# Kernel optimization log

Hardware: AMD Instinct MI355X
Metric: run time of the kernel (lower is better)

## Reference

```python
import jax, jax.numpy as jnp
import numpy as np

N, G, C, A, E = 10000, 12, 64, 3, 50000
LN_EPS = 1e-5


def setup_inputs() -> dict:
    key = jax.random.key(0)
    ks = jax.random.split(key, 12)
    s = 0.05
    return {
        "x": jax.random.normal(ks[0], (N, G, C), jnp.float32),
        "edge_attr": jax.random.normal(ks[1], (E, G, G, A), jnp.float32),
        "W_kernel": jax.random.normal(ks[2], (A, C), jnp.float32) * s,   # depthwise kernel basis Linear(attr_dim->C)
        "conv_bias": jax.random.normal(ks[3], (C,), jnp.float32) * s,
        "ln_w": jnp.ones((C,), jnp.float32),
        "ln_b": jnp.zeros((C,), jnp.float32),
        "W1": jax.random.normal(ks[4], (C, C), jnp.float32) * s,          # stored [in,out]
        "b1": jax.random.normal(ks[5], (C,), jnp.float32) * s,
        "W2": jax.random.normal(ks[6], (C, C), jnp.float32) * s,
        "b2": jax.random.normal(ks[7], (C,), jnp.float32) * s,
        "layer_scale": jnp.full((1, C), 1e-6, jnp.float32),
        "edge_index": jax.random.randint(ks[8], (2, E), 0, N, jnp.int32),
        "batch": jnp.zeros((N,), jnp.int32),
    }


def reference(x, edge_attr, W_kernel, conv_bias, ln_w, ln_b, W1, b1, W2, b2,
              layer_scale, edge_index, batch):
    src, dst = edge_index[0], edge_index[1]
    x_j = x[src]                                            # [E,G,C] gather
    # depthwise fiber conv: m[e,g,c] = sum_{h,a} attr[e,g,h,a] * Wk[a,c] * x_j[e,h,c]
    # contract over source grid h first to avoid materializing the [E,G,G,C] kernel
    t = jnp.einsum('egha,ehc->egac', edge_attr, x_j)        # [E,G,A,C]
    m = jnp.einsum('egac,ac->egc', t, W_kernel)             # [E,G,C]
    agg = jnp.zeros_like(x).at[dst].add(m) + conv_bias      # scatter-add, [N,G,C]
    # LayerNorm over channel dim
    mu = jnp.mean(agg, axis=-1, keepdims=True)
    var = jnp.mean(jnp.square(agg - mu), axis=-1, keepdims=True)
    h = (agg - mu) * jax.lax.rsqrt(var + LN_EPS) * ln_w + ln_b
    # 2-layer MLP with exact GELU (torch default)
    h = jax.nn.gelu(h @ W1 + b1, approximate=False) @ W2 + b2
    h = layer_scale * h                                     # broadcast [1,C] over [N,G,C]
    return x + h                                            # residual (same shape)
```

## Files before the change

kernel.cpp:

```cpp
#include <hip/hip_runtime.h>
#include <math.h>

#define NN 10000
#define GG 12
#define CC 64
#define AA 3
#define EE 50000
#define LN_EPS 1e-5f
#define MAXDEG 64

typedef __attribute__((ext_vector_type(4))) float f4;
typedef __attribute__((ext_vector_type(4))) short s4;

union S4U { s4 s; unsigned int w[2]; };
union I2S { int i[2]; s4 s; };

__device__ __forceinline__ s4 pack4(float k0, float k1, float k2, float k3) {
    S4U t;
    t.w[0] = __builtin_amdgcn_perm(__float_as_uint(k1), __float_as_uint(k0), 0x07060302u);
    t.w[1] = __builtin_amdgcn_perm(__float_as_uint(k3), __float_as_uint(k2), 0x07060302u);
    return t.s;
}
__device__ __forceinline__ unsigned int pack2(float a, float b) {
    return __builtin_amdgcn_perm(__float_as_uint(b), __float_as_uint(a), 0x07060302u);
}

__device__ __forceinline__ f4 mfma_bf16(s4 a, s4 b, f4 c) {
#if __has_builtin(__builtin_amdgcn_mfma_f32_16x16x16bf16_1k)
    return __builtin_amdgcn_mfma_f32_16x16x16bf16_1k(a, b, c, 0, 0, 0);
#else
    asm volatile("v_mfma_f32_16x16x16_bf16 %0, %1, %2, %0" : "+v"(c) : "v"(a), "v"(b));
    return c;
#endif
}

__global__ __launch_bounds__(256) void xpack(const float* __restrict__ x,
                                             unsigned int* __restrict__ xp,
                                             int* __restrict__ cnt) {
    const int gid = blockIdx.x * 256 + threadIdx.x;
    if (gid < NN) cnt[gid] = 0;

    const int l  = threadIdx.x & 63;
    const int n  = blockIdx.x * 4 + (threadIdx.x >> 6);
    const int lm = l & 15;
    const int lg = l >> 4;

    unsigned int d[8];
    if (lg < 3) {
        const char* xb = (const char*)(x + n * (GG * CC)) + lg * 1024 + lm * 4;
#pragma unroll
        for (int t = 0; t < 4; ++t) {
            const float v0 = *(const float*)(xb + t * 64 + 0 * 256);
            const float v1 = *(const float*)(xb + t * 64 + 1 * 256);
            const float v2 = *(const float*)(xb + t * 64 + 2 * 256);
            const float v3 = *(const float*)(xb + t * 64 + 3 * 256);
            d[2 * t]     = pack2(v0, v1);
            d[2 * t + 1] = pack2(v2, v3);
        }
    } else {
#pragma unroll
        for (int k = 0; k < 8; ++k) d[k] = 0u;
    }
    unsigned int* o = xp + (size_t)n * 512 + l * 8;
    *(uint4*)o       = make_uint4(d[0], d[1], d[2], d[3]);
    *(uint4*)(o + 4) = make_uint4(d[4], d[5], d[6], d[7]);
}

__global__ __launch_bounds__(256) void bucket_fill(const int* __restrict__ ei,
                                                   int* __restrict__ cnt,
                                                   int* __restrict__ elist) {
    int e = blockIdx.x * 256 + threadIdx.x;
    if (e < EE) {
        int src = ei[e];
        int dst = ei[EE + e];
        int pos = atomicAdd(&cnt[dst], 1);
        if (pos < MAXDEG) elist[dst * MAXDEG + pos] = e | (src << 17);
    }
}

__global__ __launch_bounds__(256) void conv_fused(
    const unsigned int* __restrict__ xp, const float* __restrict__ attr,
    const float* __restrict__ Wk,  const float* __restrict__ cb,
    const float* __restrict__ lnw, const float* __restrict__ lnb,
    const float* __restrict__ W1,  const float* __restrict__ b1,
    const float* __restrict__ W2,  const float* __restrict__ b2,
    const float* __restrict__ ls,  const float* __restrict__ x,
    const int* __restrict__ cnt,   const int* __restrict__ elist,
    float* __restrict__ out) {
    __shared__ float scratch[4][1088];

    const int l  = threadIdx.x & 63;
    const int w  = threadIdx.x >> 6;
    const int n  = blockIdx.x * 4 + w;
    const int lm = l & 15;
    const int lg = l >> 4;

    const int fbase = (lm < 12 && lg < 3) ? (lm * 36 + lg * 12) : 0;
    const int a1l   = (l < 44) ? l : 43;

    const int deg = min(cnt[n], MAXDEG);
    const int myE = elist[n * MAXDEG + l];

    float wk[3][4];
#pragma unroll
    for (int a = 0; a < 3; ++a)
#pragma unroll
        for (int t = 0; t < 4; ++t)
            wk[a][t] = Wk[a * CC + lm + 16 * t];

    f4 acc[3][4];
#pragma unroll
    for (int a = 0; a < 3; ++a)
#pragma unroll
        for (int t = 0; t < 4; ++t) acc[a][t] = (f4){0.f, 0.f, 0.f, 0.f};

    f4 Aa0, Aa1, Ab0, Ab1;
    int4 Xa0, Xa1, Xb0, Xb1;

#define LOADE(idx, A0, A1, X0, X1)                                              \
    {                                                                           \
        const int p = __builtin_amdgcn_readlane(myE, (idx));                    \
        const char* ab = (const char*)(attr + (size_t)(p & 0x1FFFF) * 432);     \
        A0 = *(const f4*)(ab + 16 * l);                                         \
        A1 = *(const f4*)(ab + 1024 + 16 * a1l);                                \
        const int* xb = (const int*)(xp + (size_t)(p >> 17) * 512 + 8 * l);     \
        X0 = *(const int4*)xb;                                                  \
        X1 = *(const int4*)(xb + 4);                                            \
    }

#define STAGE(slot, A0, A1)                                                     \
    {                                                                           \
        float* sw = &scratch[w][(slot) * 432];                                  \
        *(f4*)(sw + 4 * l) = A0;                                                \
        if (l < 44) *(f4*)(sw + 256 + 4 * l) = A1;                              \
    }

#define COMPUTE(slot, X0, X1)                                                   \
    {                                                                           \
        I2S u0, u1, u2, u3;                                                     \
        u0.i[0] = X0.x; u0.i[1] = X0.y;                                         \
        u1.i[0] = X0.z; u1.i[1] = X0.w;                                         \
        u2.i[0] = X1.x; u2.i[1] = X1.y;                                         \
        u3.i[0] = X1.z; u3.i[1] = X1.w;                                         \
        const float* sr = &scratch[w][(slot) * 432] + fbase;                    \
        const f4 q0 = *(const f4*)(sr);                                         \
        const f4 q1 = *(const f4*)(sr + 4);                                     \
        const f4 q2 = *(const f4*)(sr + 8);                                     \
        const s4 af0 = pack4(q0[0], q0[3], q1[2], q2[1]);                       \
        const s4 af1 = pack4(q0[1], q1[0], q1[3], q2[2]);                       \
        const s4 af2 = pack4(q0[2], q1[1], q2[0], q2[3]);                       \
        acc[0][0] = mfma_bf16(af0, u0.s, acc[0][0]);                            \
        acc[1][0] = mfma_bf16(af1, u0.s, acc[1][0]);                            \
        acc[2][0] = mfma_bf16(af2, u0.s, acc[2][0]);                            \
        acc[0][1] = mfma_bf16(af0, u1.s, acc[0][1]);                            \
        acc[1][1] = mfma_bf16(af1, u1.s, acc[1][1]);                            \
        acc[2][1] = mfma_bf16(af2, u1.s, acc[2][1]);                            \
        acc[0][2] = mfma_bf16(af0, u2.s, acc[0][2]);                            \
        acc[1][2] = mfma_bf16(af1, u2.s, acc[1][2]);                            \
        acc[2][2] = mfma_bf16(af2, u2.s, acc[2][2]);                            \
        acc[0][3] = mfma_bf16(af0, u3.s, acc[0][3]);                            \
        acc[1][3] = mfma_bf16(af1, u3.s, acc[1][3]);                            \
        acc[2][3] = mfma_bf16(af2, u3.s, acc[2][3]);                            \
    }

    if (deg > 0) LOADE(0, Aa0, Aa1, Xa0, Xa1);
    if (deg > 1) LOADE(1, Ab0, Ab1, Xb0, Xb1);
    if (deg > 0) STAGE(0, Aa0, Aa1);

    for (int j = 0; j < deg; j += 2) {
        COMPUTE(0, Xa0, Xa1);
        if (j + 2 < deg) LOADE(j + 2, Aa0, Aa1, Xa0, Xa1);
        if (j + 1 < deg) {
            STAGE(1, Ab0, Ab1);
            COMPUTE(1, Xb0, Xb1);
            if (j + 3 < deg) LOADE(j + 3, Ab0, Ab1, Xb0, Xb1);
            if (j + 2 < deg) STAGE(0, Aa0, Aa1);
        }
    }

#undef LOADE
#undef STAGE
#undef COMPUTE

    float* hb = &scratch[w][0];

    if (lg < 3) {
#pragma unroll
        for (int t = 0; t < 4; ++t) {
            const float cbT = cb[lm + 16 * t];
#pragma unroll
            for (int r = 0; r < 4; ++r) {
                const float mv = fmaf(acc[0][t][r], wk[0][t],
                                 fmaf(acc[1][t][r], wk[1][t],
                                      acc[2][t][r] * wk[2][t])) + cbT;
                hb[(4 * lg + r) * 68 + lm + 16 * t] = mv;
            }
        }
    }
    *(f4*)(hb + (12 + lg) * 68 + 4 * lm) = (f4){0.f, 0.f, 0.f, 0.f};

    f4 h4[4];
#pragma unroll
    for (int kt = 0; kt < 4; ++kt)
        h4[kt] = *(const f4*)(hb + lm * 68 + 4 * lg + 16 * kt);

    f4 lw4[4], lb4[4];
#pragma unroll
    for (int kt = 0; kt < 4; ++kt) {
        lw4[kt] = *(const f4*)(lnw + 4 * lg + 16 * kt);
        lb4[kt] = *(const f4*)(lnb + 4 * lg + 16 * kt);
    }

    float s = 0.f, s2 = 0.f;
#pragma unroll
    for (int kt = 0; kt < 4; ++kt)
#pragma unroll
        for (int j = 0; j < 4; ++j) {
            const float v = h4[kt][j];
            s += v; s2 += v * v;
        }
    s  += __shfl_xor(s, 16);  s  += __shfl_xor(s, 32);
    s2 += __shfl_xor(s2, 16); s2 += __shfl_xor(s2, 32);
    const float mu  = s * (1.f / 64.f);
    const float inv = rsqrtf(s2 * (1.f / 64.f) - mu * mu + LN_EPS);

    s4 hf[4];
#pragma unroll
    for (int kt = 0; kt < 4; ++kt) {
        const float n0 = (h4[kt][0] - mu) * inv * lw4[kt][0] + lb4[kt][0];
        const float n1 = (h4[kt][1] - mu) * inv * lw4[kt][1] + lb4[kt][1];
        const float n2 = (h4[kt][2] - mu) * inv * lw4[kt][2] + lb4[kt][2];
        const float n3 = (h4[kt][3] - mu) * inv * lw4[kt][3] + lb4[kt][3];
        hf[kt] = pack4(n0, n1, n2, n3);
    }

    f4 z[4];
#pragma unroll
    for (int mt = 0; mt < 4; ++mt) z[mt] = (f4){0.f, 0.f, 0.f, 0.f};
#pragma unroll
    for (int mt = 0; mt < 4; ++mt)
#pragma unroll
        for (int kt = 0; kt < 4; ++kt) {
            const int kb = 4 * lg + 16 * kt;
            const int m  = lm + 16 * mt;
            const s4 wf = pack4(W1[(kb + 0) * CC + m], W1[(kb + 1) * CC + m],
                                W1[(kb + 2) * CC + m], W1[(kb + 3) * CC + m]);
            z[mt] = mfma_bf16(wf, hf[kt], z[mt]);
        }

    s4 gf[4];
#pragma unroll
    for (int mt = 0; mt < 4; ++mt) {
        const f4 b14 = *(const f4*)(b1 + 16 * mt + 4 * lg);
        float g[4];
#pragma unroll
        for (int r = 0; r < 4; ++r) {
            const float zz = z[mt][r] + b14[r];
            g[r] = 0.5f * zz * (1.f + erff(zz * 0.70710678118654752f));
        }
        gf[mt] = pack4(g[0], g[1], g[2], g[3]);
    }

    f4 o[4];
#pragma unroll
    for (int mt = 0; mt < 4; ++mt) o[mt] = (f4){0.f, 0.f, 0.f, 0.f};
#pragma unroll
    for (int mt = 0; mt < 4; ++mt)
#pragma unroll
        for (int kt = 0; kt < 4; ++kt) {
            const int kb = 4 * lg + 16 * kt;
            const int m  = lm + 16 * mt;
            const s4 wf = pack4(W2[(kb + 0) * CC + m], W2[(kb + 1) * CC + m],
                                W2[(kb + 2) * CC + m], W2[(kb + 3) * CC + m]);
            o[mt] = mfma_bf16(wf, gf[kt], o[mt]);
        }

    const int fb2 = lm * 68;
    const int swz = (l & 7) << 2;
#pragma unroll
    for (int mt = 0; mt < 4; ++mt)
#pragma unroll
        for (int r = 0; r < 4; ++r)
            hb[fb2 + ((16 * mt + 4 * lg + r) ^ swz)] = o[mt][r];

    const f4 b2q = *(const f4*)(b2 + 4 * lm);
    const f4 lsq = *(const f4*)(ls + 4 * lm);
    const int f0 = n * GG;

#pragma unroll
    for (int rr = 0; rr < 3; ++rr) {
        const int R   = rr * 4 + lg;
        const int col = 4 * lm;
        const f4 ov = *(const f4*)(&hb[R * 68 + (col ^ ((R & 7) << 2))]);
        const f4 xv = *(const f4*)(x + (size_t)(f0 + R) * CC + col);
        f4 res;
#pragma unroll
        for (int k = 0; k < 4; ++k)
            res[k] = fmaf(lsq[k], ov[k] + b2q[k], xv[k]);
        *(f4*)(out + (size_t)(f0 + R) * CC + col) = res;
    }
}

extern "C" void kernel_launch(void* const* d_in, const int* in_sizes, int n_in,
                              void* d_out, int out_size, void* d_ws, size_t ws_size,
                              hipStream_t stream) {
    const float* x    = (const float*)d_in[0];
    const float* attr = (const float*)d_in[1];
    const float* Wk   = (const float*)d_in[2];
    const float* cb   = (const float*)d_in[3];
    const float* lnw  = (const float*)d_in[4];
    const float* lnb  = (const float*)d_in[5];
    const float* W1   = (const float*)d_in[6];
    const float* b1   = (const float*)d_in[7];
    const float* W2   = (const float*)d_in[8];
    const float* b2   = (const float*)d_in[9];
    const float* ls   = (const float*)d_in[10];
    const int*   ei   = (const int*)d_in[11];
    float* out = (float*)d_out;

    int* cnt   = (int*)d_ws;
    int* elist = cnt + NN;
    unsigned int* xp = (unsigned int*)(elist + NN * MAXDEG);

    xpack<<<NN / 4, 256, 0, stream>>>(x, xp, cnt);
    bucket_fill<<<(EE + 255) / 256, 256, 0, stream>>>(ei, cnt, elist);
    conv_fused<<<NN / 4, 256, 0, stream>>>(xp, attr, Wk, cb, lnw, lnb, W1, b1,
                                           W2, b2, ls, x, cnt, elist, out);
}
```

Before: 69.61 us.

## Sort nodes by degree for load balance and restructure edge loop into 3-edge chunks

Adds histogram, prefix and scatter kernels that build a node ordering sorted by descending in-degree. The fused conv kernel then processes nodes in that order, so the four waves in a block have similar edge counts and the heaviest nodes are scheduled first. The edge loop is also changed from a 2-stage software pipeline to chunks that issue up to three edge loads before computing. The cost is three extra small kernel launches, including a serial single-thread prefix, plus scattered output and x accesses from the permuted node order.

Measured after the change: 156.7 us. 125% more time.

```diff
diff --git a/kernel.cpp b/kernel.cpp
--- a/kernel.cpp
+++ b/kernel.cpp
@@ -36,9 +36,11 @@
 
 __global__ __launch_bounds__(256) void xpack(const float* __restrict__ x,
                                              unsigned int* __restrict__ xp,
-                                             int* __restrict__ cnt) {
+                                             int* __restrict__ cnt,
+                                             int* __restrict__ hist) {
     const int gid = blockIdx.x * 256 + threadIdx.x;
     if (gid < NN) cnt[gid] = 0;
+    if (gid < 2 * (MAXDEG + 1)) hist[gid] = 0;
 
     const int l  = threadIdx.x & 63;
     const int n  = blockIdx.x * 4 + (threadIdx.x >> 6);
@@ -78,6 +80,28 @@
     }
 }
 
+__global__ __launch_bounds__(256) void deg_hist(const int* __restrict__ cnt,
+                                                int* __restrict__ hist) {
+    int n = blockIdx.x * 256 + threadIdx.x;
+    if (n < NN) atomicAdd(&hist[min(cnt[n], MAXDEG)], 1);
+}
+__global__ __launch_bounds__(64) void deg_prefix(const int* __restrict__ hist,
+                                                 int* __restrict__ off) {
+    if (threadIdx.x == 0) {
+        int acc = 0;
+        for (int d = MAXDEG; d >= 0; --d) { off[d] = acc; acc += hist[d]; }
+    }
+}
+__global__ __launch_bounds__(256) void deg_scatter(const int* __restrict__ cnt,
+                                                   int* __restrict__ off,
+                                                   int* __restrict__ nord) {
+    int n = blockIdx.x * 256 + threadIdx.x;
+    if (n < NN) {
+        int pos = atomicAdd(&off[min(cnt[n], MAXDEG)], 1);
+        nord[pos] = n;
+    }
+}
+
 __global__ __launch_bounds__(256) void conv_fused(
     const unsigned int* __restrict__ xp, const float* __restrict__ attr,
     const float* __restrict__ Wk,  const float* __restrict__ cb,
@@ -86,12 +110,13 @@
     const float* __restrict__ W2,  const float* __restrict__ b2,
     const float* __restrict__ ls,  const float* __restrict__ x,
     const int* __restrict__ cnt,   const int* __restrict__ elist,
+    const int* __restrict__ nord,
     float* __restrict__ out) {
     __shared__ float scratch[4][1088];
 
     const int l  = threadIdx.x & 63;
     const int w  = threadIdx.x >> 6;
-    const int n  = blockIdx.x * 4 + w;
+    const int n  = nord[blockIdx.x * 4 + w];
     const int lm = l & 15;
     const int lg = l >> 4;
 
@@ -114,8 +139,8 @@
 #pragma unroll
         for (int t = 0; t < 4; ++t) acc[a][t] = (f4){0.f, 0.f, 0.f, 0.f};
 
-    f4 Aa0, Aa1, Ab0, Ab1;
-    int4 Xa0, Xa1, Xb0, Xb1;
+    f4 Aa0, Aa1, Ab0, Ab1, Ac0, Ac1;
+    int4 Xa0, Xa1, Xb0, Xb1, Xc0, Xc1;
 
 #define LOADE(idx, A0, A1, X0, X1)                                              \
     {                                                                           \
@@ -163,24 +188,31 @@
         acc[2][3] = mfma_bf16(af2, u3.s, acc[2][3]);                            \
     }
 
-    if (deg > 0) LOADE(0, Aa0, Aa1, Xa0, Xa1);
-    if (deg > 1) LOADE(1, Ab0, Ab1, Xb0, Xb1);
-    if (deg > 0) STAGE(0, Aa0, Aa1);
-
-    for (int j = 0; j < deg; j += 2) {
-        COMPUTE(0, Xa0, Xa1);
-        if (j + 2 < deg) LOADE(j + 2, Aa0, Aa1, Xa0, Xa1);
-        if (j + 1 < deg) {
-            STAGE(1, Ab0, Ab1);
-            COMPUTE(1, Xb0, Xb1);
-            if (j + 3 < deg) LOADE(j + 3, Ab0, Ab1, Xb0, Xb1);
-            if (j + 2 < deg) STAGE(0, Aa0, Aa1);
-        }
+#define CH1(i) { LOADE((i),Aa0,Aa1,Xa0,Xa1);                                    \
+                 STAGE(0,Aa0,Aa1); COMPUTE(0,Xa0,Xa1); }
+#define CH2(i) { LOADE((i),Aa0,Aa1,Xa0,Xa1); LOADE((i)+1,Ab0,Ab1,Xb0,Xb1);      \
+                 STAGE(0,Aa0,Aa1); COMPUTE(0,Xa0,Xa1);                          \
+                 STAGE(1,Ab0,Ab1); COMPUTE(1,Xb0,Xb1); }
+#define CH3(i) { LOADE((i),Aa0,Aa1,Xa0,Xa1); LOADE((i)+1,Ab0,Ab1,Xb0,Xb1);      \
+                 LOADE((i)+2,Ac0,Ac1,Xc0,Xc1);                                  \
+                 STAGE(0,Aa0,Aa1); COMPUTE(0,Xa0,Xa1);                          \
+                 STAGE(1,Ab0,Ab1); COMPUTE(1,Xb0,Xb1);                          \
+                 STAGE(0,Ac0,Ac1); COMPUTE(0,Xc0,Xc1); }
+
+    int i = 0;
+    while (i < deg) {
+        const int c = deg - i;
+        if (c >= 3)      { CH3(i); i += 3; }
+        else if (c == 2) { CH2(i); i += 2; }
+        else             { CH1(i); i += 1; }
     }
 
 #undef LOADE
 #undef STAGE
 #undef COMPUTE
+#undef CH1
+#undef CH2
+#undef CH3
 
     float* hb = &scratch[w][0];
 
@@ -321,9 +353,15 @@
     int* cnt   = (int*)d_ws;
     int* elist = cnt + NN;
     unsigned int* xp = (unsigned int*)(elist + NN * MAXDEG);
-
-    xpack<<<NN / 4, 256, 0, stream>>>(x, xp, cnt);
+    int* hist  = (int*)(xp + (size_t)NN * 512);
+    int* off   = hist + (MAXDEG + 1);
+    int* nord  = off + (MAXDEG + 1);
+
+    xpack<<<NN / 4, 256, 0, stream>>>(x, xp, cnt, hist);
     bucket_fill<<<(EE + 255) / 256, 256, 0, stream>>>(ei, cnt, elist);
+    deg_hist<<<(NN + 255) / 256, 256, 0, stream>>>(cnt, hist);
+    deg_prefix<<<1, 64, 0, stream>>>(hist, off);
+    deg_scatter<<<(NN + 255) / 256, 256, 0, stream>>>(cnt, off, nord);
     conv_fused<<<NN / 4, 256, 0, stream>>>(xp, attr, Wk, cb, lnw, lnb, W1, b1,
-                                           W2, b2, ls, x, cnt, elist, out);
-}
+                                           W2, b2, ls, x, cnt, elist, nord, out);
+}
```

## Stream edge attr and packed x directly to LDS with triple-buffered async loads

Applied to the files above, without the earlier changes.

Replaces the register-staged double-buffered gather (global loads into VGPRs, then ds_write to LDS) with global_load_lds direct-to-LDS copies into a three-slot ring per wave. The loop paces itself with explicit vmcnt waits and prefetches up to three edges ahead. The aim is to drop the VGPR round-trip and LDS store instructions and to hide gather latency with deeper prefetch. In exchange, LDS per block grows from about 17 KB to 48 KB, which may lower occupancy, and correctness now relies on hand-written waitcnt counts matching the number of issued loads.

Measured after the change: 69.83 us. Within noise of the previous version (+0.3%).

```diff
diff --git a/kernel.cpp b/kernel.cpp
--- a/kernel.cpp
+++ b/kernel.cpp
@@ -32,6 +32,12 @@
     asm volatile("v_mfma_f32_16x16x16_bf16 %0, %1, %2, %0" : "+v"(c) : "v"(a), "v"(b));
     return c;
 #endif
+}
+
+__device__ __forceinline__ void gll(const void* g, void* s) {
+    __builtin_amdgcn_global_load_lds(
+        (const __attribute__((address_space(1))) void*)g,
+        (__attribute__((address_space(3))) void*)s, 16, 0, 0);
 }
 
 __global__ __launch_bounds__(256) void xpack(const float* __restrict__ x,
@@ -87,7 +93,7 @@
     const float* __restrict__ ls,  const float* __restrict__ x,
     const int* __restrict__ cnt,   const int* __restrict__ elist,
     float* __restrict__ out) {
-    __shared__ float scratch[4][1088];
+    __shared__ float lsa[4][3][1024];
 
     const int l  = threadIdx.x & 63;
     const int w  = threadIdx.x >> 6;
@@ -101,6 +107,73 @@
     const int deg = min(cnt[n], MAXDEG);
     const int myE = elist[n * MAXDEG + l];
 
+    f4 acc[3][4];
+#pragma unroll
+    for (int a = 0; a < 3; ++a)
+#pragma unroll
+        for (int t = 0; t < 4; ++t) acc[a][t] = (f4){0.f, 0.f, 0.f, 0.f};
+
+#define ISSUE(idx, s)                                                           \
+    {                                                                           \
+        const int p = __builtin_amdgcn_readlane(myE, (idx));                    \
+        const char* ab = (const char*)attr + (size_t)(p & 0x1FFFF) * 1728;      \
+        const char* xb = (const char*)xp + (size_t)(p >> 17) * 2048;            \
+        char* sw = (char*)&lsa[w][s][0];                                        \
+        gll(ab + 16 * l,            sw);                                        \
+        gll(ab + 1024 + 16 * a1l,   sw + 1024);                                 \
+        gll(xb + 32 * l,            sw + 2048);                                 \
+        gll(xb + 32 * l + 16,       sw + 3072);                                 \
+    }
+
+    if (deg > 0) ISSUE(0, 0);
+    if (deg > 1) ISSUE(1, 1);
+    if (deg > 2) ISSUE(2, 2);
+
+    int s = 0;
+    for (int i = 0; i < deg; ++i) {
+        const int ahead = deg - 1 - i;
+        if (ahead >= 2)      asm volatile("s_waitcnt vmcnt(8)" ::: "memory");
+        else if (ahead == 1) asm volatile("s_waitcnt vmcnt(4)" ::: "memory");
+        else                 asm volatile("s_waitcnt vmcnt(0)" ::: "memory");
+        __builtin_amdgcn_sched_barrier(0);
+
+        const float* sr = &lsa[w][s][0];
+        const f4 q0 = *(const f4*)(sr + fbase);
+        const f4 q1 = *(const f4*)(sr + fbase + 4);
+        const f4 q2 = *(const f4*)(sr + fbase + 8);
+        const int4 X0 = *(const int4*)((const char*)sr + 2048 + 16 * l);
+        const int4 X1 = *(const int4*)((const char*)sr + 3072 + 16 * l);
+
+        asm volatile("s_waitcnt lgkmcnt(0)" ::: "memory");
+        __builtin_amdgcn_sched_barrier(0);
+        if (i + 3 < deg) ISSUE(i + 3, s);
+
+        I2S u0, u1, u2, u3;
+        u0.i[0] = X0.x; u0.i[1] = X0.y;
+        u1.i[0] = X0.z; u1.i[1] = X0.w;
+        u2.i[0] = X1.x; u2.i[1] = X1.y;
+        u3.i[0] = X1.z; u3.i[1] = X1.w;
+        const s4 af0 = pack4(q0[0], q0[3], q1[2], q2[1]);
+        const s4 af1 = pack4(q0[1], q1[0], q1[3], q2[2]);
+        const s4 af2 = pack4(q0[2], q1[1], q2[0], q2[3]);
+        acc[0][0] = mfma_bf16(af0, u0.s, acc[0][0]);
+        acc[1][0] = mfma_bf16(af1, u0.s, acc[1][0]);
+        acc[2][0] = mfma_bf16(af2, u0.s, acc[2][0]);
+        acc[0][1] = mfma_bf16(af0, u1.s, acc[0][1]);
+        acc[1][1] = mfma_bf16(af1, u1.s, acc[1][1]);
+        acc[2][1] = mfma_bf16(af2, u1.s, acc[2][1]);
+        acc[0][2] = mfma_bf16(af0, u2.s, acc[0][2]);
+        acc[1][2] = mfma_bf16(af1, u2.s, acc[1][2]);
+        acc[2][2] = mfma_bf16(af2, u2.s, acc[2][2]);
+        acc[0][3] = mfma_bf16(af0, u3.s, acc[0][3]);
+        acc[1][3] = mfma_bf16(af1, u3.s, acc[1][3]);
+        acc[2][3] = mfma_bf16(af2, u3.s, acc[2][3]);
+
+        s = (s == 2) ? 0 : s + 1;
+    }
+
+#undef ISSUE
+
     float wk[3][4];
 #pragma unroll
     for (int a = 0; a < 3; ++a)
@@ -108,81 +181,7 @@
         for (int t = 0; t < 4; ++t)
             wk[a][t] = Wk[a * CC + lm + 16 * t];
 
-    f4 acc[3][4];
-#pragma unroll
-    for (int a = 0; a < 3; ++a)
-#pragma unroll
-        for (int t = 0; t < 4; ++t) acc[a][t] = (f4){0.f, 0.f, 0.f, 0.f};
-
-    f4 Aa0, Aa1, Ab0, Ab1;
-    int4 Xa0, Xa1, Xb0, Xb1;
-
-#define LOADE(idx, A0, A1, X0, X1)                                              \
-    {                                                                           \
-        const int p = __builtin_amdgcn_readlane(myE, (idx));                    \
-        const char* ab = (const char*)(attr + (size_t)(p & 0x1FFFF) * 432);     \
-        A0 = *(const f4*)(ab + 16 * l);                                         \
-        A1 = *(const f4*)(ab + 1024 + 16 * a1l);                                \
-        const int* xb = (const int*)(xp + (size_t)(p >> 17) * 512 + 8 * l);     \
-        X0 = *(const int4*)xb;                                                  \
-        X1 = *(const int4*)(xb + 4);                                            \
-    }
-
-#define STAGE(slot, A0, A1)                                                     \
-    {                                                                           \
-        float* sw = &scratch[w][(slot) * 432];                                  \
-        *(f4*)(sw + 4 * l) = A0;                                                \
-        if (l < 44) *(f4*)(sw + 256 + 4 * l) = A1;                              \
-    }
-
-#define COMPUTE(slot, X0, X1)                                                   \
-    {                                                                           \
-        I2S u0, u1, u2, u3;                                                     \
-        u0.i[0] = X0.x; u0.i[1] = X0.y;                                         \
-        u1.i[0] = X0.z; u1.i[1] = X0.w;                                         \
-        u2.i[0] = X1.x; u2.i[1] = X1.y;                                         \
-        u3.i[0] = X1.z; u3.i[1] = X1.w;                                         \
-        const float* sr = &scratch[w][(slot) * 432] + fbase;                    \
-        const f4 q0 = *(const f4*)(sr);                                         \
-        const f4 q1 = *(const f4*)(sr + 4);                                     \
-        const f4 q2 = *(const f4*)(sr + 8);                                     \
-        const s4 af0 = pack4(q0[0], q0[3], q1[2], q2[1]);                       \
-        const s4 af1 = pack4(q0[1], q1[0], q1[3], q2[2]);                       \
-        const s4 af2 = pack4(q0[2], q1[1], q2[0], q2[3]);                       \
-        acc[0][0] = mfma_bf16(af0, u0.s, acc[0][0]);                            \
-        acc[1][0] = mfma_bf16(af1, u0.s, acc[1][0]);                            \
-        acc[2][0] = mfma_bf16(af2, u0.s, acc[2][0]);                            \
-        acc[0][1] = mfma_bf16(af0, u1.s, acc[0][1]);                            \
-        acc[1][1] = mfma_bf16(af1, u1.s, acc[1][1]);                            \
-        acc[2][1] = mfma_bf16(af2, u1.s, acc[2][1]);                            \
-        acc[0][2] = mfma_bf16(af0, u2.s, acc[0][2]);                            \
-        acc[1][2] = mfma_bf16(af1, u2.s, acc[1][2]);                            \
-        acc[2][2] = mfma_bf16(af2, u2.s, acc[2][2]);                            \
-        acc[0][3] = mfma_bf16(af0, u3.s, acc[0][3]);                            \
-        acc[1][3] = mfma_bf16(af1, u3.s, acc[1][3]);                            \
-        acc[2][3] = mfma_bf16(af2, u3.s, acc[2][3]);                            \
-    }
-
-    if (deg > 0) LOADE(0, Aa0, Aa1, Xa0, Xa1);
-    if (deg > 1) LOADE(1, Ab0, Ab1, Xb0, Xb1);
-    if (deg > 0) STAGE(0, Aa0, Aa1);
-
-    for (int j = 0; j < deg; j += 2) {
-        COMPUTE(0, Xa0, Xa1);
-        if (j + 2 < deg) LOADE(j + 2, Aa0, Aa1, Xa0, Xa1);
-        if (j + 1 < deg) {
-            STAGE(1, Ab0, Ab1);
-            COMPUTE(1, Xb0, Xb1);
-            if (j + 3 < deg) LOADE(j + 3, Ab0, Ab1, Xb0, Xb1);
-            if (j + 2 < deg) STAGE(0, Aa0, Aa1);
-        }
-    }
-
-#undef LOADE
-#undef STAGE
-#undef COMPUTE
-
-    float* hb = &scratch[w][0];
+    float* hb = &lsa[w][0][0];
 
     if (lg < 3) {
 #pragma unroll
@@ -211,17 +210,17 @@
         lb4[kt] = *(const f4*)(lnb + 4 * lg + 16 * kt);
     }
 
-    float s = 0.f, s2 = 0.f;
+    float s1 = 0.f, s2 = 0.f;
 #pragma unroll
     for (int kt = 0; kt < 4; ++kt)
 #pragma unroll
         for (int j = 0; j < 4; ++j) {
             const float v = h4[kt][j];
-            s += v; s2 += v * v;
-        }
-    s  += __shfl_xor(s, 16);  s  += __shfl_xor(s, 32);
+            s1 += v; s2 += v * v;
+        }
+    s1 += __shfl_xor(s1, 16); s1 += __shfl_xor(s1, 32);
     s2 += __shfl_xor(s2, 16); s2 += __shfl_xor(s2, 32);
-    const float mu  = s * (1.f / 64.f);
+    const float mu  = s1 * (1.f / 64.f);
     const float inv = rsqrtf(s2 * (1.f / 64.f) - mu * mu + LN_EPS);
 
     s4 hf[4];
```

## Stream edge attrs via global_load_lds with 4-deep pipeline and prepacked MLP weights

Applied to the files above, without the earlier changes.

Edge attribute rows are now loaded straight into LDS with global_load_lds into a 5-slot ring per wave. The gather loop is restructured to keep four edges in flight, using explicit vmcnt waits, which removes the register staging and the LDS write pass. MLP weights are packed to bf16 MFMA fragments once, inside bucket_fill, so conv_fused reads ready fragments instead of repacking strided fp32 loads in every block. The change also sets a launch_bounds occupancy hint and raises LDS use to 40KB per block, which may limit occupancy. The hand-coded vmcnt counts depend on the exact number of memory ops each ISSUE emits, so correctness rests on that count.

Measured after the change: 74.50 us. 1.07x slower.

```diff
diff --git a/kernel.cpp b/kernel.cpp
--- a/kernel.cpp
+++ b/kernel.cpp
@@ -34,6 +34,12 @@
 #endif
 }
 
+__device__ __forceinline__ void gll(const void* g, void* s) {
+    __builtin_amdgcn_global_load_lds(
+        (const __attribute__((address_space(1))) void*)g,
+        (__attribute__((address_space(3))) void*)s, 16, 0, 0);
+}
+
 __global__ __launch_bounds__(256) void xpack(const float* __restrict__ x,
                                              unsigned int* __restrict__ xp,
                                              int* __restrict__ cnt) {
@@ -68,7 +74,10 @@
 
 __global__ __launch_bounds__(256) void bucket_fill(const int* __restrict__ ei,
                                                    int* __restrict__ cnt,
-                                                   int* __restrict__ elist) {
+                                                   int* __restrict__ elist,
+                                                   const float* __restrict__ W1,
+                                                   const float* __restrict__ W2,
+                                                   char* __restrict__ wtab) {
     int e = blockIdx.x * 256 + threadIdx.x;
     if (e < EE) {
         int src = ei[e];
@@ -76,18 +85,33 @@
         int pos = atomicAdd(&cnt[dst], 1);
         if (pos < MAXDEG) elist[dst * MAXDEG + pos] = e | (src << 17);
     }
-}
-
-__global__ __launch_bounds__(256) void conv_fused(
+    if (blockIdx.x < 2) {
+        const float* Ws = (blockIdx.x == 0) ? W1 : W2;
+        char* base = wtab + blockIdx.x * 8192;
+        const int l  = threadIdx.x & 63;
+        const int wv = threadIdx.x >> 6;
+        const int lm = l & 15, lg = l >> 4;
+        const int m  = lm + 16 * wv;
+#pragma unroll
+        for (int kt = 0; kt < 4; ++kt) {
+            const int kb = 4 * lg + 16 * kt;
+            const s4 f = pack4(Ws[(kb + 0) * CC + m], Ws[(kb + 1) * CC + m],
+                               Ws[(kb + 2) * CC + m], Ws[(kb + 3) * CC + m]);
+            *(s4*)(base + (wv * 4 + kt) * 512 + l * 8) = f;
+        }
+    }
+}
+
+__global__ __launch_bounds__(256, 4) void conv_fused(
     const unsigned int* __restrict__ xp, const float* __restrict__ attr,
     const float* __restrict__ Wk,  const float* __restrict__ cb,
     const float* __restrict__ lnw, const float* __restrict__ lnb,
-    const float* __restrict__ W1,  const float* __restrict__ b1,
-    const float* __restrict__ W2,  const float* __restrict__ b2,
-    const float* __restrict__ ls,  const float* __restrict__ x,
+    const char* __restrict__ wtab, const float* __restrict__ b1,
+    const float* __restrict__ b2,  const float* __restrict__ ls,
+    const float* __restrict__ x,
     const int* __restrict__ cnt,   const int* __restrict__ elist,
     float* __restrict__ out) {
-    __shared__ float scratch[4][1088];
+    __shared__ float lsa[4][5][512];
 
     const int l  = threadIdx.x & 63;
     const int w  = threadIdx.x >> 6;
@@ -101,51 +125,44 @@
     const int deg = min(cnt[n], MAXDEG);
     const int myE = elist[n * MAXDEG + l];
 
-    float wk[3][4];
+    f4 acc[3][4];
 #pragma unroll
     for (int a = 0; a < 3; ++a)
 #pragma unroll
-        for (int t = 0; t < 4; ++t)
-            wk[a][t] = Wk[a * CC + lm + 16 * t];
-
-    f4 acc[3][4];
-#pragma unroll
-    for (int a = 0; a < 3; ++a)
-#pragma unroll
         for (int t = 0; t < 4; ++t) acc[a][t] = (f4){0.f, 0.f, 0.f, 0.f};
 
-    f4 Aa0, Aa1, Ab0, Ab1;
-    int4 Xa0, Xa1, Xb0, Xb1;
-
-#define LOADE(idx, A0, A1, X0, X1)                                              \
+    int4 Xa0, Xa1, Xb0, Xb1, Xc0, Xc1, Xd0, Xd1;
+
+#define ISSUE(idx, X0, X1)                                                      \
     {                                                                           \
         const int p = __builtin_amdgcn_readlane(myE, (idx));                    \
-        const char* ab = (const char*)(attr + (size_t)(p & 0x1FFFF) * 432);     \
-        A0 = *(const f4*)(ab + 16 * l);                                         \
-        A1 = *(const f4*)(ab + 1024 + 16 * a1l);                                \
+        const char* ab = (const char*)attr + (size_t)(p & 0x1FFFF) * 1728;      \
         const int* xb = (const int*)(xp + (size_t)(p >> 17) * 512 + 8 * l);     \
+        char* sw = (char*)&lsa[w][(idx) % 5][0];                                \
+        gll(ab + 16 * l,          sw);                                          \
+        gll(ab + 1024 + 16 * a1l, sw + 1024);                                   \
         X0 = *(const int4*)xb;                                                  \
         X1 = *(const int4*)(xb + 4);                                            \
     }
 
-#define STAGE(slot, A0, A1)                                                     \
+#define EDGE(e, X0, X1)                                                         \
     {                                                                           \
-        float* sw = &scratch[w][(slot) * 432];                                  \
-        *(f4*)(sw + 4 * l) = A0;                                                \
-        if (l < 44) *(f4*)(sw + 256 + 4 * l) = A1;                              \
-    }
-
-#define COMPUTE(slot, X0, X1)                                                   \
-    {                                                                           \
+        const int ahead = deg - 1 - (e);                                        \
+        if (ahead >= 3)      asm volatile("s_waitcnt vmcnt(12)" ::: "memory");  \
+        else if (ahead == 2) asm volatile("s_waitcnt vmcnt(8)" ::: "memory");   \
+        else if (ahead == 1) asm volatile("s_waitcnt vmcnt(4)" ::: "memory");   \
+        else                 asm volatile("s_waitcnt vmcnt(0)" ::: "memory");   \
+        __builtin_amdgcn_sched_barrier(0);                                      \
+        const float* sr = &lsa[w][(e) % 5][0];                                  \
+        const f4 q0 = *(const f4*)(sr + fbase);                                 \
+        const f4 q1 = *(const f4*)(sr + fbase + 4);                             \
+        const f4 q2 = *(const f4*)(sr + fbase + 8);                             \
         I2S u0, u1, u2, u3;                                                     \
         u0.i[0] = X0.x; u0.i[1] = X0.y;                                         \
         u1.i[0] = X0.z; u1.i[1] = X0.w;                                         \
         u2.i[0] = X1.x; u2.i[1] = X1.y;                                         \
         u3.i[0] = X1.z; u3.i[1] = X1.w;                                         \
-        const float* sr = &scratch[w][(slot) * 432] + fbase;                    \
-        const f4 q0 = *(const f4*)(sr);                                         \
-        const f4 q1 = *(const f4*)(sr + 4);                                     \
-        const f4 q2 = *(const f4*)(sr + 8);                                     \
+        if ((e) + 4 < deg) ISSUE((e) + 4, X0, X1);                              \
         const s4 af0 = pack4(q0[0], q0[3], q1[2], q2[1]);                       \
         const s4 af1 = pack4(q0[1], q1[0], q1[3], q2[2]);                       \
         const s4 af2 = pack4(q0[2], q1[1], q2[0], q2[3]);                       \
@@ -163,26 +180,39 @@
         acc[2][3] = mfma_bf16(af2, u3.s, acc[2][3]);                            \
     }
 
-    if (deg > 0) LOADE(0, Aa0, Aa1, Xa0, Xa1);
-    if (deg > 1) LOADE(1, Ab0, Ab1, Xb0, Xb1);
-    if (deg > 0) STAGE(0, Aa0, Aa1);
-
-    for (int j = 0; j < deg; j += 2) {
-        COMPUTE(0, Xa0, Xa1);
-        if (j + 2 < deg) LOADE(j + 2, Aa0, Aa1, Xa0, Xa1);
-        if (j + 1 < deg) {
-            STAGE(1, Ab0, Ab1);
-            COMPUTE(1, Xb0, Xb1);
-            if (j + 3 < deg) LOADE(j + 3, Ab0, Ab1, Xb0, Xb1);
-            if (j + 2 < deg) STAGE(0, Aa0, Aa1);
-        }
-    }
-
-#undef LOADE
-#undef STAGE
-#undef COMPUTE
-
-    float* hb = &scratch[w][0];
+    if (deg > 0) ISSUE(0, Xa0, Xa1);
+    if (deg > 1) ISSUE(1, Xb0, Xb1);
+    if (deg > 2) ISSUE(2, Xc0, Xc1);
+    if (deg > 3) ISSUE(3, Xd0, Xd1);
+
+    int i = 0;
+    for (; i + 4 <= deg; i += 4) {
+        EDGE(i,     Xa0, Xa1);
+        EDGE(i + 1, Xb0, Xb1);
+        EDGE(i + 2, Xc0, Xc1);
+        EDGE(i + 3, Xd0, Xd1);
+    }
+    if (i < deg) {
+        EDGE(i, Xa0, Xa1);
+        if (i + 1 < deg) {
+            EDGE(i + 1, Xb0, Xb1);
+            if (i + 2 < deg) {
+                EDGE(i + 2, Xc0, Xc1);
+            }
+        }
+    }
+
+#undef ISSUE
+#undef EDGE
+
+    float wk[3][4];
+#pragma unroll
+    for (int a = 0; a < 3; ++a)
+#pragma unroll
+        for (int t = 0; t < 4; ++t)
+            wk[a][t] = Wk[a * CC + lm + 16 * t];
+
+    float* hb = &lsa[w][0][0];
 
     if (lg < 3) {
 #pragma unroll
@@ -211,17 +241,17 @@
         lb4[kt] = *(const f4*)(lnb + 4 * lg + 16 * kt);
     }
 
-    float s = 0.f, s2 = 0.f;
+    float s1 = 0.f, s2 = 0.f;
 #pragma unroll
     for (int kt = 0; kt < 4; ++kt)
 #pragma unroll
         for (int j = 0; j < 4; ++j) {
             const float v = h4[kt][j];
-            s += v; s2 += v * v;
-        }
-    s  += __shfl_xor(s, 16);  s  += __shfl_xor(s, 32);
+            s1 += v; s2 += v * v;
+        }
+    s1 += __shfl_xor(s1, 16); s1 += __shfl_xor(s1, 32);
     s2 += __shfl_xor(s2, 16); s2 += __shfl_xor(s2, 32);
-    const float mu  = s * (1.f / 64.f);
+    const float mu  = s1 * (1.f / 64.f);
     const float inv = rsqrtf(s2 * (1.f / 64.f) - mu * mu + LN_EPS);
 
     s4 hf[4];
@@ -234,6 +264,7 @@
         hf[kt] = pack4(n0, n1, n2, n3);
     }
 
+    const char* wt = wtab + l * 8;
     f4 z[4];
 #pragma unroll
     for (int mt = 0; mt < 4; ++mt) z[mt] = (f4){0.f, 0.f, 0.f, 0.f};
@@ -241,10 +272,7 @@
     for (int mt = 0; mt < 4; ++mt)
 #pragma unroll
         for (int kt = 0; kt < 4; ++kt) {
-            const int kb = 4 * lg + 16 * kt;
-            const int m  = lm + 16 * mt;
-            const s4 wf = pack4(W1[(kb + 0) * CC + m], W1[(kb + 1) * CC + m],
-                                W1[(kb + 2) * CC + m], W1[(kb + 3) * CC + m]);
+            const s4 wf = *(const s4*)(wt + (mt * 4 + kt) * 512);
             z[mt] = mfma_bf16(wf, hf[kt], z[mt]);
         }
 
@@ -268,10 +296,7 @@
     for (int mt = 0; mt < 4; ++mt)
 #pragma unroll
         for (int kt = 0; kt < 4; ++kt) {
-            const int kb = 4 * lg + 16 * kt;
-            const int m  = lm + 16 * mt;
-            const s4 wf = pack4(W2[(kb + 0) * CC + m], W2[(kb + 1) * CC + m],
-                                W2[(kb + 2) * CC + m], W2[(kb + 3) * CC + m]);
+            const s4 wf = *(const s4*)(wt + 8192 + (mt * 4 + kt) * 512);
             o[mt] = mfma_bf16(wf, gf[kt], o[mt]);
         }
 
@@ -321,9 +346,10 @@
     int* cnt   = (int*)d_ws;
     int* elist = cnt + NN;
     unsigned int* xp = (unsigned int*)(elist + NN * MAXDEG);
+    char* wtab = (char*)(xp + (size_t)NN * 512);
 
     xpack<<<NN / 4, 256, 0, stream>>>(x, xp, cnt);
-    bucket_fill<<<(EE + 255) / 256, 256, 0, stream>>>(ei, cnt, elist);
-    conv_fused<<<NN / 4, 256, 0, stream>>>(xp, attr, Wk, cb, lnw, lnb, W1, b1,
-                                           W2, b2, ls, x, cnt, elist, out);
-}
+    bucket_fill<<<(EE + 255) / 256, 256, 0, stream>>>(ei, cnt, elist, W1, W2, wtab);
+    conv_fused<<<NN / 4, 256, 0, stream>>>(xp, attr, Wk, cb, lnw, lnb, wtab, b1,
+                                           b2, ls, x, cnt, elist, out);
+}
```
